# Performance work log

Measured on AMD Instinct MI355X. Metric: run time of the kernel, lower is better.

## Reference

```python
import jax, jax.numpy as jnp
import numpy as np

B, T, E = 64, 2048, 1024

def setup_inputs() -> dict:
    key = jax.random.key(0)
    k1, k2, k3, k4 = jax.random.split(key, 4)
    x = jax.random.normal(k1, (B, T, E), dtype=jnp.float32)
    c = jax.random.normal(k2, (B, E), dtype=jnp.float32)
    W = jax.random.normal(k3, (E, 1), dtype=jnp.float32) * 0.05
    b = jnp.zeros((T, 1), dtype=jnp.float32)
    U = jax.random.normal(k4, (E, T), dtype=jnp.float32) * 0.05
    return {"x": x, "c": c, "W": W, "b": b, "U": U}

def reference(x, c, W, b, U):
    # et: (B,T) = c @ U + squeeze(x @ W + b, -1)
    et = jnp.einsum('be,et->bt', c, U) + (jnp.einsum('bte,eo->bto', x, W) + b)[..., 0]
    at = jax.nn.softmax(et, axis=-1)                 # (B,T)
    # weighted sum over timesteps -> (B,E)
    return jnp.einsum('bt,bte->be', at, x)
```

## Files before the change

kernel.cpp:

```cpp
#include <hip/hip_runtime.h>
#include <stdint.h>

#define BB 64
#define TT 2048
#define EE 1024
#define ST 32
#define TBLK (TT / ST)
#define BG 2
#define NBG (BB / BG)
#define RPP 4
#define NPH (BG * TBLK / RPP)

#define S_OFF 0
#define O_OFF 2048

typedef float f32x4v __attribute__((ext_vector_type(4)));
__device__ __forceinline__ float4 ntload4(const float4* p) {
    f32x4v v = __builtin_nontemporal_load((const f32x4v*)p);
    float4 r; r.x = v[0]; r.y = v[1]; r.z = v[2]; r.w = v[3]; return r;
}
__device__ __forceinline__ void ntstore4(float4* p, float4 d) {
    f32x4v v; v[0] = d.x; v[1] = d.y; v[2] = d.z; v[3] = d.w;
    __builtin_nontemporal_store(v, (f32x4v*)p);
}

#define PHASE(ph, CUR, NXT)                                                    \
  do {                                                                         \
    if ((ph) + 2 < NPH) {                                                      \
      const int bl1 = ((ph) + 2) >> 4, tl1 = (((ph) + 2) & 15) * RPP;          \
      const float4* srcp = xq + ((size_t)bl1 * TT + tl1) * 256;                \
      _Pragma("unroll")                                                        \
      for (int r = 0; r < 4; ++r) NXT[r] = ntload4(srcp + (size_t)r * 256);    \
    }                                                                          \
    float s_[4];                                                               \
    _Pragma("unroll")                                                          \
    for (int r = 0; r < 4; ++r)                                                \
      s_[r] = CUR[r].x * wf.x + CUR[r].y * wf.y +                              \
              CUR[r].z * wf.z + CUR[r].w * wf.w;                               \
                        \
    float t_[2];                                                               \
    _Pragma("unroll")                                                          \
    for (int r = 0; r < 2; ++r) {                                              \
      const float ar = s_[r]     + __shfl_xor(s_[r],     32, 64);              \
      const float br = s_[r + 2] + __shfl_xor(s_[r + 2], 32, 64);              \
      t_[r] = (lane < 32) ? ar : br;                                           \
    }                                                                          \
                                 \
    float u_;                                                                  \
    {                                                                          \
      const float ar = t_[0] + __shfl_xor(t_[0], 16, 64);                      \
      const float br = t_[1] + __shfl_xor(t_[1], 16, 64);                      \
      u_ = ((lane & 16) == 0) ? ar : br;                                       \
    }                                                                          \
    u_ += __shfl_xor(u_, 8, 64);                                               \
    u_ += __shfl_xor(u_, 4, 64);                                               \
    u_ += __shfl_xor(u_, 2, 64);                                               \
    u_ += __shfl_xor(u_, 1, 64);                                               \
    if ((lane & 15) == 0) ex[(ph) & 1][lane >> 4][wu] = u_;                    \
    asm volatile("s_waitcnt lgkmcnt(0)" ::: "memory");                         \
    __builtin_amdgcn_s_barrier();                                              \
    asm volatile("" ::: "memory");                                             \
    const int bl_ = (ph) >> 4, tl_ = ((ph) & 15) * RPP;                        \
    const float4 cu4 = *(const float4*)&cu_s[bl_][tl_];                        \
    float et[4];                                                               \
    _Pragma("unroll")                                                          \
    for (int r = 0; r < 4; ++r) {                                              \
      const float4 q = ((const float4*)ex[(ph) & 1])[r];   \
      et[r] = (q.x + q.y) + (q.z + q.w);                                       \
    }                                                                          \
    et[0] += cu4.x; et[1] += cu4.y; et[2] += cu4.z; et[3] += cu4.w;            \
    float p_[4];                                                               \
    _Pragma("unroll")                                                          \
    for (int r = 0; r < 4; ++r) p_[r] = __expf(et[r]);                         \
    l += (p_[0] + p_[1]) + (p_[2] + p_[3]);                                    \
    _Pragma("unroll")                                                          \
    for (int r = 0; r < 4; ++r) {                                              \
      o.x = fmaf(p_[r], CUR[r].x, o.x); o.y = fmaf(p_[r], CUR[r].y, o.y);      \
      o.z = fmaf(p_[r], CUR[r].z, o.z); o.w = fmaf(p_[r], CUR[r].w, o.w);      \
    }                                                                          \
    if (((ph) & 15) == 15) {                                                   \
      const int pi = (b0 + bl_) * ST + ts;                                     \
      ntstore4(((float4*)O_part) + (size_t)pi * 256 + (wu << 6) + lane, o);    \
      if (tid == 0) S_part[pi] = l;                                            \
      l = 0.f; o = make_float4(0.f, 0.f, 0.f, 0.f);                            \
    }                                                                          \
  } while (0)

__global__ __launch_bounds__(256, 4) void k_fused(
    const float* __restrict__ x, const float* __restrict__ c,
    const float* __restrict__ W, const float* __restrict__ bvec,
    const float* __restrict__ U,
    float* __restrict__ S_part, float* __restrict__ O_part)
{
    const int bg   = blockIdx.x >> 5;
    const int ts   = blockIdx.x & 31;
    const int b0   = bg * BG;
    const int t0   = ts * TBLK;
    const int tid  = threadIdx.x;
    const int wu   = __builtin_amdgcn_readfirstlane(tid >> 6);
    const int lane = tid & 63;

    __shared__ float cu_s[BG][TBLK];
    __shared__ float pcu[4][BG][TBLK];
    __shared__ float ex[2][4][4];

    const float4* xq = (const float4*)x + ((size_t)b0 * TT + t0) * 256 + (wu << 6) + lane;

    float4 XA[4], XB[4], XC[4];
    #pragma unroll
    for (int r = 0; r < 4; ++r) XA[r] = ntload4(xq + (size_t)r * 256);
    #pragma unroll
    for (int r = 0; r < 4; ++r) XB[r] = ntload4(xq + (size_t)(RPP + r) * 256);

    {
        const float* cb = c + (size_t)b0 * EE + (wu << 8);
        const float* Ub = U + ((size_t)(wu << 8)) * TT + t0 + lane;
        float a0 = 0.f, a1 = 0.f;
        #pragma unroll 8
        for (int e = 0; e < 256; ++e) {
            const float u = Ub[(size_t)e * TT];
            a0 = fmaf(cb[e], u, a0);
            a1 = fmaf(cb[EE + e], u, a1);
        }
        pcu[wu][0][lane] = a0;
        pcu[wu][1][lane] = a1;
    }
    __syncthreads();
    if (tid < BG * TBLK) {
        const int j = tid >> 6, t = tid & 63;
        cu_s[j][t] = bvec[t0 + t] + pcu[0][j][t] + pcu[1][j][t] + pcu[2][j][t] + pcu[3][j][t];
    }
    __syncthreads();

    const float4 wf = ((const float4*)W)[(wu << 6) + lane];
    float  l = 0.f;
    float4 o = make_float4(0.f, 0.f, 0.f, 0.f);

    for (int ph = 0; ph < NPH - 2; ph += 3) {
        PHASE(ph,     XA, XC);
        PHASE(ph + 1, XB, XA);
        PHASE(ph + 2, XC, XB);
    }
    PHASE(NPH - 2, XA, XC);
    PHASE(NPH - 1, XB, XA);
}

__global__ __launch_bounds__(256) void k_merge(const float* __restrict__ S_part,
                                               const float* __restrict__ O_part,
                                               float* __restrict__ out) {
    const int b  = blockIdx.x >> 2;
    const int eq = blockIdx.x & 3;
    const int e  = eq * 256 + threadIdx.x;

    float S = 0.f, acc = 0.f;
    #pragma unroll 4
    for (int p = 0; p < ST; ++p) {
        const int pi = b * ST + p;
        S   += S_part[pi];
        acc += O_part[(size_t)pi * EE + e];
    }
    out[(size_t)b * EE + e] = acc / S;
}

extern "C" void kernel_launch(void* const* d_in, const int* in_sizes, int n_in,
                              void* d_out, int out_size, void* d_ws, size_t ws_size,
                              hipStream_t stream) {
    const float* x    = (const float*)d_in[0];
    const float* c    = (const float*)d_in[1];
    const float* W    = (const float*)d_in[2];
    const float* bvec = (const float*)d_in[3];
    const float* U    = (const float*)d_in[4];
    float* out = (float*)d_out;

    float* ws     = (float*)d_ws;
    float* S_part = ws + S_OFF;
    float* O_part = ws + O_OFF;

    k_fused<<<NBG * ST, 256, 0, stream>>>(x, c, W, bvec, U, S_part, O_part);
    k_merge<<<BB * 4, 256, 0, stream>>>(S_part, O_part, out);
}
```

Baseline: 105.5 us.

## Split c@U projection into separate kernel and simplify fused block mapping

Moves the c·U + b projection out of the fused streaming kernel into its own kernel that writes a (B,T) buffer to workspace. The fused kernel now handles one batch row per block with 16 time splits instead of two rows with 32 splits, so each block has a contiguous x stream and writes a single partial at the end. The goal is to take the strided U reads and the extra barriers off the critical path of the bandwidth-bound x stream. In exchange it adds a kernel launch and a round trip of the cu buffer through global memory. The merge kernel gains an unused pointer.

```diff
diff --git a/kernel.cpp b/kernel.cpp
--- a/kernel.cpp
+++ b/kernel.cpp
@@ -4,15 +4,14 @@
 #define BB 64
 #define TT 2048
 #define EE 1024
-#define ST 32
+#define ST 16
 #define TBLK (TT / ST)
-#define BG 2
-#define NBG (BB / BG)
 #define RPP 4
-#define NPH (BG * TBLK / RPP)
+#define NPH (TBLK / RPP)
 
-#define S_OFF 0
-#define O_OFF 2048
+#define CU_OFF 0
+#define S_OFF  (BB * TT)
+#define O_OFF  (S_OFF + 1024)
 
 typedef float f32x4v __attribute__((ext_vector_type(4)));
 __device__ __forceinline__ float4 ntload4(const float4* p) {
@@ -27,8 +26,7 @@
 #define PHASE(ph, CUR, NXT)                                                    \
   do {                                                                         \
     if ((ph) + 2 < NPH) {                                                      \
-      const int bl1 = ((ph) + 2) >> 4, tl1 = (((ph) + 2) & 15) * RPP;          \
-      const float4* srcp = xq + ((size_t)bl1 * TT + tl1) * 256;                \
+      const float4* srcp = xq + (size_t)((ph) + 2) * (RPP * 256);              \
       _Pragma("unroll")                                                        \
       for (int r = 0; r < 4; ++r) NXT[r] = ntload4(srcp + (size_t)r * 256);    \
     }                                                                          \
@@ -60,8 +58,7 @@
     asm volatile("s_waitcnt lgkmcnt(0)" ::: "memory");                         \
     __builtin_amdgcn_s_barrier();                                              \
     asm volatile("" ::: "memory");                                             \
-    const int bl_ = (ph) >> 4, tl_ = ((ph) & 15) * RPP;                        \
-    const float4 cu4 = *(const float4*)&cu_s[bl_][tl_];                        \
+    const float4 cu4 = *(const float4*)&cu_s[RPP * (ph)];                      \
     float et[4];                                                               \
     _Pragma("unroll")                                                          \
     for (int r = 0; r < 4; ++r) {                                              \
@@ -78,33 +75,45 @@
       o.x = fmaf(p_[r], CUR[r].x, o.x); o.y = fmaf(p_[r], CUR[r].y, o.y);      \
       o.z = fmaf(p_[r], CUR[r].z, o.z); o.w = fmaf(p_[r], CUR[r].w, o.w);      \
     }                                                                          \
-    if (((ph) & 15) == 15) {                                                   \
-      const int pi = (b0 + bl_) * ST + ts;                                     \
-      ntstore4(((float4*)O_part) + (size_t)pi * 256 + (wu << 6) + lane, o);    \
-      if (tid == 0) S_part[pi] = l;                                            \
-      l = 0.f; o = make_float4(0.f, 0.f, 0.f, 0.f);                            \
-    }                                                                          \
   } while (0)
 
+__global__ __launch_bounds__(256) void k_cu(const float* __restrict__ c,
+                                            const float* __restrict__ bvec,
+                                            const float* __restrict__ U,
+                                            float* __restrict__ cu) {
+    const int tch = blockIdx.x & 7;
+    const int b   = blockIdx.x >> 3;
+    const int t   = tch * 256 + threadIdx.x;
+
+    const float* cb = c + (size_t)b * EE;
+    const float* Up = U + t;
+    float a0 = 0.f, a1 = 0.f, a2 = 0.f, a3 = 0.f;
+    #pragma unroll 4
+    for (int e = 0; e < EE; e += 4) {
+        a0 = fmaf(cb[e + 0], Up[(size_t)(e + 0) * TT], a0);
+        a1 = fmaf(cb[e + 1], Up[(size_t)(e + 1) * TT], a1);
+        a2 = fmaf(cb[e + 2], Up[(size_t)(e + 2) * TT], a2);
+        a3 = fmaf(cb[e + 3], Up[(size_t)(e + 3) * TT], a3);
+    }
+    cu[(size_t)b * TT + t] = bvec[t] + (a0 + a1) + (a2 + a3);
+}
+
 __global__ __launch_bounds__(256, 4) void k_fused(
-    const float* __restrict__ x, const float* __restrict__ c,
-    const float* __restrict__ W, const float* __restrict__ bvec,
-    const float* __restrict__ U,
+    const float* __restrict__ x, const float* __restrict__ cu,
+    const float* __restrict__ W,
     float* __restrict__ S_part, float* __restrict__ O_part)
 {
-    const int bg   = blockIdx.x >> 5;
-    const int ts   = blockIdx.x & 31;
-    const int b0   = bg * BG;
+    const int b    = blockIdx.x >> 4;
+    const int ts   = blockIdx.x & 15;
     const int t0   = ts * TBLK;
     const int tid  = threadIdx.x;
     const int wu   = __builtin_amdgcn_readfirstlane(tid >> 6);
     const int lane = tid & 63;
 
-    __shared__ float cu_s[BG][TBLK];
-    __shared__ float pcu[4][BG][TBLK];
+    __shared__ float cu_s[TBLK];
     __shared__ float ex[2][4][4];
 
-    const float4* xq = (const float4*)x + ((size_t)b0 * TT + t0) * 256 + (wu << 6) + lane;
+    const float4* xq = (const float4*)x + ((size_t)b * TT + t0) * 256 + (wu << 6) + lane;
 
     float4 XA[4], XB[4], XC[4];
     #pragma unroll
@@ -112,24 +121,7 @@
     #pragma unroll
     for (int r = 0; r < 4; ++r) XB[r] = ntload4(xq + (size_t)(RPP + r) * 256);
 
-    {
-        const float* cb = c + (size_t)b0 * EE + (wu << 8);
-        const float* Ub = U + ((size_t)(wu << 8)) * TT + t0 + lane;
-        float a0 = 0.f, a1 = 0.f;
-        #pragma unroll 8
-        for (int e = 0; e < 256; ++e) {
-            const float u = Ub[(size_t)e * TT];
-            a0 = fmaf(cb[e], u, a0);
-            a1 = fmaf(cb[EE + e], u, a1);
-        }
-        pcu[wu][0][lane] = a0;
-        pcu[wu][1][lane] = a1;
-    }
-    __syncthreads();
-    if (tid < BG * TBLK) {
-        const int j = tid >> 6, t = tid & 63;
-        cu_s[j][t] = bvec[t0 + t] + pcu[0][j][t] + pcu[1][j][t] + pcu[2][j][t] + pcu[3][j][t];
-    }
+    if (tid < TBLK) cu_s[tid] = cu[(size_t)b * TT + t0 + tid];
     __syncthreads();
 
     const float4 wf = ((const float4*)W)[(wu << 6) + lane];
@@ -143,6 +135,10 @@
     }
     PHASE(NPH - 2, XA, XC);
     PHASE(NPH - 1, XB, XA);
+
+    const int pi = blockIdx.x;
+    ntstore4(((float4*)O_part) + (size_t)pi * 256 + (wu << 6) + lane, o);
+    if (tid == 0) S_part[pi] = l;
 }
 
 __global__ __launch_bounds__(256) void k_merge(const float* __restrict__ S_part,
@@ -152,11 +148,13 @@
     const int eq = blockIdx.x & 3;
     const int e  = eq * 256 + threadIdx.x;
 
-    float S = 0.f, acc = 0.f;
+    float S = 0.f;
+    float acc = 0.f;
     #pragma unroll 4
     for (int p = 0; p < ST; ++p) {
         const int pi = b * ST + p;
-        S   += S_part[pi];
+        S += S_part[pi];
+        const float4* op = (const float4*)(O_part + (size_t)pi * EE) + (e >> 2);
         acc += O_part[(size_t)pi * EE + e];
     }
     out[(size_t)b * EE + e] = acc / S;
@@ -173,9 +171,11 @@
     float* out = (float*)d_out;
 
     float* ws     = (float*)d_ws;
+    float* cu     = ws + CU_OFF;
     float* S_part = ws + S_OFF;
     float* O_part = ws + O_OFF;
 
-    k_fused<<<NBG * ST, 256, 0, stream>>>(x, c, W, bvec, U, S_part, O_part);
+    k_cu<<<BB * 8, 256, 0, stream>>>(c, bvec, U, cu);
+    k_fused<<<BB * ST, 256, 0, stream>>>(x, cu, W, S_part, O_part);
     k_merge<<<BB * 4, 256, 0, stream>>>(S_part, O_part, out);
 }
```

New measurement: 180.4 us. 1.71x slower.
